# Performance work log

Measured on AMD Instinct MI355X. Metric: run time of the kernel, lower is better.

## Reference

```python
import jax, jax.numpy as jnp
import numpy as np

B, N, F, C = 8, 4096, 1024, 64


def setup_inputs() -> dict:
    key = jax.random.key(0)
    k1, k2, k3 = jax.random.split(key, 3)
    x1 = jax.random.normal(k1, (B, N, F), dtype=jnp.float32)
    x2 = jax.random.normal(k2, (B, N, F), dtype=jnp.float32)
    W = jax.random.normal(k3, (C, F), dtype=jnp.float32) / np.sqrt(F)
    b = jnp.zeros((C,), dtype=jnp.float32)
    return {"x1": x1, "x2": x2, "W": W, "b": b}


def _select_max(x, W, b):
    # x: [B, N, F] -> scores [B, N, C]
    scores = jnp.einsum("bnf,cf->bnc", x, W) + b
    # per-batch, per-class index of max-scoring instance: [B, C]
    idx = jnp.argmax(scores, axis=1)
    # gather the selected instance feature vectors: [B, C, F]
    return jnp.take_along_axis(x, idx[:, :, None], axis=1)


def reference(x1, x2, W, b):
    d = _select_max(x1, W, b)
    d1 = _select_max(x2, W, b)
    return (d, d1)
```

## Files before the change

kernel.cpp:

```cpp
#include <hip/hip_runtime.h>

#define B_   8
#define N_   4096
#define F_   1024
#define C_   64
#define TN   128
#define KC   64
#define NB   (N_ / TN)
#define MARGIN 0.02f

typedef __attribute__((ext_vector_type(8))) short bhalf8;
typedef __attribute__((ext_vector_type(4))) float f32x4;
typedef __attribute__((ext_vector_type(4))) unsigned short us4;

__device__ __forceinline__ unsigned short f2bf_rne(float x) {
    unsigned u = __builtin_bit_cast(unsigned, x);
    u += 0x7fffu + ((u >> 16) & 1u);
    return (unsigned short)(u >> 16);
}
__device__ __forceinline__ float bf2f(unsigned short h) {
    unsigned u = ((unsigned)h) << 16;
    return __builtin_bit_cast(float, u);
}

#define LEXGT(a, ai, b, bi) ((a) > (b) || ((a) == (b) && (ai) < (bi)))
#define INSERT3(vv, nn)                                                   \
    do {                                                                  \
        float _v = (vv); int _n = (nn);                                   \
        if (LEXGT(_v, _n, v0, i0)) { v2=v1; i2=i1; v1=v0; i1=i0; v0=_v; i0=_n; } \
        else if (LEXGT(_v, _n, v1, i1)) { v2=v1; i2=i1; v1=_v; i1=_n; }   \
        else if (LEXGT(_v, _n, v2, i2)) { v2=_v; i2=_n; }                 \
    } while (0)

__global__ __launch_bounds__(256, 2) void score_top3_kernel(
    const float* __restrict__ x1, const float* __restrict__ x2,
    const float* __restrict__ W,
    float* __restrict__ pv, int* __restrict__ pi)
{
    __shared__ __align__(16) char lds[49152];
    __shared__ float tv[4][C_][3];
    __shared__ int   ti[4][C_][3];

    const int tid  = threadIdx.x;
    const int nb   = blockIdx.x;
    const int b    = blockIdx.y;
    const int inp  = blockIdx.z;
    const int n0   = nb * TN;
    const float* __restrict__ x = inp ? x2 : x1;
    const float* __restrict__ xbase = x + ((size_t)b * N_ + n0) * F_;

    const int lane = tid & 63;
    const int w    = tid >> 6;
    const int rsel = lane & 15;
    const int g    = lane >> 4;
    const int swz  = (rsel & 7) << 4;

    f32x4 acc[2][4];
    #pragma unroll
    for (int mt = 0; mt < 2; ++mt)
        #pragma unroll
        for (int nt = 0; nt < 4; ++nt) acc[mt][nt] = (f32x4){0.f, 0.f, 0.f, 0.f};

    for (int kc = 0; kc < F_ / KC; ++kc) {
        const int f0 = kc * KC;
        float4 xv[8], wv[4];
        #pragma unroll
        for (int j = 0; j < 8; ++j) {
            int li = tid + 256 * j, row = li >> 4, fq = li & 15;
            xv[j] = *(const float4*)(xbase + (size_t)row * F_ + f0 + fq * 4);
        }
        #pragma unroll
        for (int j = 0; j < 4; ++j) {
            int li = tid + 256 * j, c = li >> 4, fq = li & 15;
            wv[j] = *(const float4*)(W + (size_t)c * F_ + f0 + fq * 4);
        }
        #pragma unroll
        for (int j = 0; j < 8; ++j) {
            int li = tid + 256 * j, row = li >> 4, fq = li & 15;
            float f[4] = {xv[j].x, xv[j].y, xv[j].z, xv[j].w};
            us4 hh, ll;
            #pragma unroll
            for (int e = 0; e < 4; ++e) {
                unsigned short h = f2bf_rne(f[e]);
                hh[e] = h;
                ll[e] = f2bf_rne(f[e] - bf2f(h));
            }
            int off = (row * 128 + fq * 8) ^ ((row & 7) << 4);
            *(us4*)(lds + off)         = hh;
            *(us4*)(lds + 16384 + off) = ll;
        }
        #pragma unroll
        for (int j = 0; j < 4; ++j) {
            int li = tid + 256 * j, c = li >> 4, fq = li & 15;
            float f[4] = {wv[j].x, wv[j].y, wv[j].z, wv[j].w};
            us4 hh, ll;
            #pragma unroll
            for (int e = 0; e < 4; ++e) {
                unsigned short h = f2bf_rne(f[e]);
                hh[e] = h;
                ll[e] = f2bf_rne(f[e] - bf2f(h));
            }
            int off = (c * 128 + fq * 8) ^ ((c & 7) << 4);
            *(us4*)(lds + 32768 + off) = hh;
            *(us4*)(lds + 40960 + off) = ll;
        }
        __syncthreads();

        #pragma unroll
        for (int ks = 0; ks < 2; ++ks) {
            bhalf8 ah[2], al[2], bh[4], bl[4];
            #pragma unroll
            for (int mt = 0; mt < 2; ++mt) {
                int arow = w * 32 + mt * 16 + rsel;
                int off = (arow * 128 + ks * 64 + g * 16) ^ swz;
                ah[mt] = *(const bhalf8*)(lds + off);
                al[mt] = *(const bhalf8*)(lds + 16384 + off);
            }
            #pragma unroll
            for (int nt = 0; nt < 4; ++nt) {
                int brow = nt * 16 + rsel;
                int off = (brow * 128 + ks * 64 + g * 16) ^ swz;
                bh[nt] = *(const bhalf8*)(lds + 32768 + off);
                bl[nt] = *(const bhalf8*)(lds + 40960 + off);
            }
            #pragma unroll
            for (int mt = 0; mt < 2; ++mt)
                #pragma unroll
                for (int nt = 0; nt < 4; ++nt) {
                    acc[mt][nt] = __builtin_amdgcn_mfma_f32_16x16x32_bf16(ah[mt], bh[nt], acc[mt][nt], 0, 0, 0);
                    acc[mt][nt] = __builtin_amdgcn_mfma_f32_16x16x32_bf16(ah[mt], bl[nt], acc[mt][nt], 0, 0, 0);
                    acc[mt][nt] = __builtin_amdgcn_mfma_f32_16x16x32_bf16(al[mt], bh[nt], acc[mt][nt], 0, 0, 0);
                }
        }
        __syncthreads();
    }

    #pragma unroll
    for (int nt = 0; nt < 4; ++nt) {
        float v0 = -3.4e38f, v1 = -3.4e38f, v2 = -3.4e38f;
        int   i0 = 0x7fffffff, i1 = 0x7fffffff, i2 = 0x7fffffff;
        #pragma unroll
        for (int mt = 0; mt < 2; ++mt)
            #pragma unroll
            for (int r = 0; r < 4; ++r) {
                int n = n0 + w * 32 + mt * 16 + 4 * g + r;
                INSERT3(acc[mt][nt][r], n);
            }
        #pragma unroll
        for (int d = 16; d <= 32; d <<= 1) {
            float u0 = __shfl_xor(v0, d), u1 = __shfl_xor(v1, d), u2 = __shfl_xor(v2, d);
            int   j0 = __shfl_xor(i0, d), j1 = __shfl_xor(i1, d), j2 = __shfl_xor(i2, d);
            INSERT3(u0, j0); INSERT3(u1, j1); INSERT3(u2, j2);
        }
        if (lane < 16) {
            int c = nt * 16 + lane;
            tv[w][c][0] = v0; tv[w][c][1] = v1; tv[w][c][2] = v2;
            ti[w][c][0] = i0; ti[w][c][1] = i1; ti[w][c][2] = i2;
        }
    }
    __syncthreads();

    if (tid < C_) {
        int c = tid;
        float v0 = tv[0][c][0], v1 = tv[0][c][1], v2 = tv[0][c][2];
        int   i0 = ti[0][c][0], i1 = ti[0][c][1], i2 = ti[0][c][2];
        #pragma unroll
        for (int ww = 1; ww < 4; ++ww) {
            INSERT3(tv[ww][c][0], ti[ww][c][0]);
            INSERT3(tv[ww][c][1], ti[ww][c][1]);
            INSERT3(tv[ww][c][2], ti[ww][c][2]);
        }
        int blk = ((inp * B_ + b) * NB + nb);
        pv[(blk * C_ + c) * 3 + 0] = v0; pi[(blk * C_ + c) * 3 + 0] = i0;
        pv[(blk * C_ + c) * 3 + 1] = v1; pi[(blk * C_ + c) * 3 + 1] = i1;
        pv[(blk * C_ + c) * 3 + 2] = v2; pi[(blk * C_ + c) * 3 + 2] = i2;
    }
}

__global__ __launch_bounds__(256) void select_gather_kernel(
    const float* __restrict__ x1, const float* __restrict__ x2,
    const float* __restrict__ W,
    const float* __restrict__ pv, const int* __restrict__ pi,
    float* __restrict__ out)
{
    const int c   = blockIdx.x;
    const int b   = blockIdx.y;
    const int inp = blockIdx.z;
    const int tid = threadIdx.x;

    __shared__ int   s_cnt;
    __shared__ int   s_cand[8];
    __shared__ float s_val[8];
    __shared__ float s_wsum[4];
    __shared__ int   s_win;

    if (tid == 0) s_cnt = 0;
    __syncthreads();

    if (tid < 64) {
        float m = -3.4e38f;
        if (tid < 32) {
            int blk = ((inp * B_ + b) * NB + tid);
            m = pv[(blk * C_ + c) * 3 + 0];
        }
        #pragma unroll
        for (int d = 32; d; d >>= 1) m = fmaxf(m, __shfl_xor(m, d));
        if (tid < 32) {
            int blk = ((inp * B_ + b) * NB + tid);
            #pragma unroll
            for (int k = 0; k < 3; ++k) {
                float v = pv[(blk * C_ + c) * 3 + k];
                if (v >= m - MARGIN) {
                    int p = atomicAdd(&s_cnt, 1);
                    if (p < 8) s_cand[p] = pi[(blk * C_ + c) * 3 + k];
                }
            }
        }
    }
    __syncthreads();

    const float* __restrict__ x = inp ? x2 : x1;
    const int ncand = min(s_cnt, 8);
    int winner;
    if (ncand == 1) {
        winner = s_cand[0];
    } else {
        for (int k = 0; k < ncand; ++k) {
            int n = s_cand[k];
            float4 xv = *(const float4*)(x + ((size_t)b * N_ + n) * F_ + tid * 4);
            float4 wv = *(const float4*)(W + (size_t)c * F_ + tid * 4);
            float p = xv.x * wv.x + xv.y * wv.y + xv.z * wv.z + xv.w * wv.w;
            #pragma unroll
            for (int d = 32; d; d >>= 1) p += __shfl_down(p, d);
            if ((tid & 63) == 0) s_wsum[tid >> 6] = p;
            __syncthreads();
            if (tid == 0) s_val[k] = s_wsum[0] + s_wsum[1] + s_wsum[2] + s_wsum[3];
            __syncthreads();
        }
        if (tid == 0) {
            float bv = s_val[0]; int bn = s_cand[0];
            for (int k = 1; k < ncand; ++k)
                if (s_val[k] > bv || (s_val[k] == bv && s_cand[k] < bn)) { bv = s_val[k]; bn = s_cand[k]; }
            s_win = bn;
        }
        __syncthreads();
        winner = s_win;
    }

    float4 v = *(const float4*)(x + ((size_t)b * N_ + winner) * F_ + tid * 4);
    *(float4*)(out + (((size_t)inp * B_ + b) * C_ + c) * F_ + tid * 4) = v;
}

extern "C" void kernel_launch(void* const* d_in, const int* in_sizes, int n_in,
                              void* d_out, int out_size, void* d_ws, size_t ws_size,
                              hipStream_t stream) {
    const float* x1 = (const float*)d_in[0];
    const float* x2 = (const float*)d_in[1];
    const float* W  = (const float*)d_in[2];

    float* pv = (float*)d_ws;
    int*   pi = (int*)((char*)d_ws + (size_t)2 * B_ * NB * C_ * 3 * sizeof(float));

    dim3 g1(NB, B_, 2);
    score_top3_kernel<<<g1, 256, 0, stream>>>(x1, x2, W, pv, pi);
    dim3 g2(C_, B_, 2);
    select_gather_kernel<<<g2, 256, 0, stream>>>(x1, x2, W, pv, pi, (float*)d_out);
}
```

Baseline: 70.95 us.

## Precompute split-bf16 W, halve row tile, prefetch next x chunk in registers

Adds a small pre-kernel that converts W into hi/lo bf16 arrays once, so the score kernel reads B fragments straight from global memory instead of converting and staging W in LDS for every block. The row tile drops from 128 to 64 and LDS shrinks to 32 KB, allowing 4 blocks per CU. The next K-chunk of x is loaded into registers while the current MFMAs run, overlapping global loads with compute. Per-block candidates drop from top-3 to top-2, which relies on the smaller tile to keep candidate recall. The cost is an extra kernel launch and W fragment reads from global or cache in every block.

```diff
diff --git a/kernel.cpp b/kernel.cpp
--- a/kernel.cpp
+++ b/kernel.cpp
@@ -4,7 +4,7 @@
 #define N_   4096
 #define F_   1024
 #define C_   64
-#define TN   128
+#define TN   64
 #define KC   64
 #define NB   (N_ / TN)
 #define MARGIN 0.02f
@@ -24,22 +24,37 @@
 }
 
 #define LEXGT(a, ai, b, bi) ((a) > (b) || ((a) == (b) && (ai) < (bi)))
-#define INSERT3(vv, nn)                                                   \
+#define INSERT2(vv, nn)                                                   \
     do {                                                                  \
         float _v = (vv); int _n = (nn);                                   \
-        if (LEXGT(_v, _n, v0, i0)) { v2=v1; i2=i1; v1=v0; i1=i0; v0=_v; i0=_n; } \
-        else if (LEXGT(_v, _n, v1, i1)) { v2=v1; i2=i1; v1=_v; i1=_n; }   \
-        else if (LEXGT(_v, _n, v2, i2)) { v2=_v; i2=_n; }                 \
+        if (LEXGT(_v, _n, v0, i0)) { v1=v0; i1=i0; v0=_v; i0=_n; }        \
+        else if (LEXGT(_v, _n, v1, i1)) { v1=_v; i1=_n; }                 \
     } while (0)
 
-__global__ __launch_bounds__(256, 2) void score_top3_kernel(
+__global__ __launch_bounds__(256) void wconv_kernel(
+    const float* __restrict__ W,
+    unsigned short* __restrict__ Wh, unsigned short* __restrict__ Wl)
+{
+    int i = blockIdx.x * 256 + threadIdx.x;
+    float4 v = ((const float4*)W)[i];
+    float f[4] = {v.x, v.y, v.z, v.w};
+    us4 hh, ll;
+    #pragma unroll
+    for (int e = 0; e < 4; ++e) {
+        unsigned short h = f2bf_rne(f[e]);
+        hh[e] = h;
+        ll[e] = f2bf_rne(f[e] - bf2f(h));
+    }
+    ((us4*)Wh)[i] = hh;
+    ((us4*)Wl)[i] = ll;
+}
+
+__global__ __launch_bounds__(256, 4) void score_top2_kernel(
     const float* __restrict__ x1, const float* __restrict__ x2,
-    const float* __restrict__ W,
+    const unsigned short* __restrict__ Wh, const unsigned short* __restrict__ Wl,
     float* __restrict__ pv, int* __restrict__ pi)
 {
-    __shared__ __align__(16) char lds[49152];
-    __shared__ float tv[4][C_][3];
-    __shared__ int   ti[4][C_][3];
+    __shared__ __align__(16) char lds[32768];
 
     const int tid  = threadIdx.x;
     const int nb   = blockIdx.x;
@@ -55,27 +70,20 @@
     const int g    = lane >> 4;
     const int swz  = (rsel & 7) << 4;
 
-    f32x4 acc[2][4];
-    #pragma unroll
-    for (int mt = 0; mt < 2; ++mt)
-        #pragma unroll
-        for (int nt = 0; nt < 4; ++nt) acc[mt][nt] = (f32x4){0.f, 0.f, 0.f, 0.f};
+    f32x4 acc[4];
+    #pragma unroll
+    for (int nt = 0; nt < 4; ++nt) acc[nt] = (f32x4){0.f, 0.f, 0.f, 0.f};
+
+    float4 xv[4];
+    #pragma unroll
+    for (int j = 0; j < 4; ++j) {
+        int li = tid + 256 * j, row = li >> 4, fq = li & 15;
+        xv[j] = *(const float4*)(xbase + (size_t)row * F_ + fq * 4);
+    }
 
     for (int kc = 0; kc < F_ / KC; ++kc) {
-        const int f0 = kc * KC;
-        float4 xv[8], wv[4];
-        #pragma unroll
-        for (int j = 0; j < 8; ++j) {
-            int li = tid + 256 * j, row = li >> 4, fq = li & 15;
-            xv[j] = *(const float4*)(xbase + (size_t)row * F_ + f0 + fq * 4);
-        }
         #pragma unroll
         for (int j = 0; j < 4; ++j) {
-            int li = tid + 256 * j, c = li >> 4, fq = li & 15;
-            wv[j] = *(const float4*)(W + (size_t)c * F_ + f0 + fq * 4);
-        }
-        #pragma unroll
-        for (int j = 0; j < 8; ++j) {
             int li = tid + 256 * j, row = li >> 4, fq = li & 15;
             float f[4] = {xv[j].x, xv[j].y, xv[j].z, xv[j].w};
             us4 hh, ll;
@@ -89,91 +97,81 @@
             *(us4*)(lds + off)         = hh;
             *(us4*)(lds + 16384 + off) = ll;
         }
-        #pragma unroll
-        for (int j = 0; j < 4; ++j) {
-            int li = tid + 256 * j, c = li >> 4, fq = li & 15;
-            float f[4] = {wv[j].x, wv[j].y, wv[j].z, wv[j].w};
-            us4 hh, ll;
-            #pragma unroll
-            for (int e = 0; e < 4; ++e) {
-                unsigned short h = f2bf_rne(f[e]);
-                hh[e] = h;
-                ll[e] = f2bf_rne(f[e] - bf2f(h));
-            }
-            int off = (c * 128 + fq * 8) ^ ((c & 7) << 4);
-            *(us4*)(lds + 32768 + off) = hh;
-            *(us4*)(lds + 40960 + off) = ll;
-        }
         __syncthreads();
 
+        bhalf8 ah[2], al[2];
         #pragma unroll
         for (int ks = 0; ks < 2; ++ks) {
-            bhalf8 ah[2], al[2], bh[4], bl[4];
-            #pragma unroll
-            for (int mt = 0; mt < 2; ++mt) {
-                int arow = w * 32 + mt * 16 + rsel;
-                int off = (arow * 128 + ks * 64 + g * 16) ^ swz;
-                ah[mt] = *(const bhalf8*)(lds + off);
-                al[mt] = *(const bhalf8*)(lds + 16384 + off);
-            }
+            int arow = w * 16 + rsel;
+            int off = (arow * 128 + ks * 64 + g * 16) ^ swz;
+            ah[ks] = *(const bhalf8*)(lds + off);
+            al[ks] = *(const bhalf8*)(lds + 16384 + off);
+        }
+        bhalf8 bh[2][4], bl[2][4];
+        #pragma unroll
+        for (int ks = 0; ks < 2; ++ks)
             #pragma unroll
             for (int nt = 0; nt < 4; ++nt) {
-                int brow = nt * 16 + rsel;
-                int off = (brow * 128 + ks * 64 + g * 16) ^ swz;
-                bh[nt] = *(const bhalf8*)(lds + 32768 + off);
-                bl[nt] = *(const bhalf8*)(lds + 40960 + off);
-            }
-            #pragma unroll
-            for (int mt = 0; mt < 2; ++mt)
-                #pragma unroll
-                for (int nt = 0; nt < 4; ++nt) {
-                    acc[mt][nt] = __builtin_amdgcn_mfma_f32_16x16x32_bf16(ah[mt], bh[nt], acc[mt][nt], 0, 0, 0);
-                    acc[mt][nt] = __builtin_amdgcn_mfma_f32_16x16x32_bf16(ah[mt], bl[nt], acc[mt][nt], 0, 0, 0);
-                    acc[mt][nt] = __builtin_amdgcn_mfma_f32_16x16x32_bf16(al[mt], bh[nt], acc[mt][nt], 0, 0, 0);
-                }
-        }
+                size_t off = (size_t)(nt * 16 + rsel) * F_ + kc * KC + ks * 32 + g * 8;
+                bh[ks][nt] = *(const bhalf8*)(Wh + off);
+                bl[ks][nt] = *(const bhalf8*)(Wl + off);
+            }
+        if (kc + 1 < F_ / KC) {
+            const int f0 = (kc + 1) * KC;
+            #pragma unroll
+            for (int j = 0; j < 4; ++j) {
+                int li = tid + 256 * j, row = li >> 4, fq = li & 15;
+                xv[j] = *(const float4*)(xbase + (size_t)row * F_ + f0 + fq * 4);
+            }
+        }
+        #pragma unroll
+        for (int ks = 0; ks < 2; ++ks)
+            #pragma unroll
+            for (int nt = 0; nt < 4; ++nt) {
+                acc[nt] = __builtin_amdgcn_mfma_f32_16x16x32_bf16(ah[ks], bh[ks][nt], acc[nt], 0, 0, 0);
+                acc[nt] = __builtin_amdgcn_mfma_f32_16x16x32_bf16(ah[ks], bl[ks][nt], acc[nt], 0, 0, 0);
+                acc[nt] = __builtin_amdgcn_mfma_f32_16x16x32_bf16(al[ks], bh[ks][nt], acc[nt], 0, 0, 0);
+            }
         __syncthreads();
     }
 
+    float* tv = (float*)lds;
+    int*   ti = (int*)(lds + 8192);
     #pragma unroll
     for (int nt = 0; nt < 4; ++nt) {
-        float v0 = -3.4e38f, v1 = -3.4e38f, v2 = -3.4e38f;
-        int   i0 = 0x7fffffff, i1 = 0x7fffffff, i2 = 0x7fffffff;
-        #pragma unroll
-        for (int mt = 0; mt < 2; ++mt)
-            #pragma unroll
-            for (int r = 0; r < 4; ++r) {
-                int n = n0 + w * 32 + mt * 16 + 4 * g + r;
-                INSERT3(acc[mt][nt][r], n);
-            }
+        float v0 = -3.4e38f, v1 = -3.4e38f;
+        int   i0 = 0x7fffffff, i1 = 0x7fffffff;
+        #pragma unroll
+        for (int r = 0; r < 4; ++r) {
+            int n = n0 + w * 16 + 4 * g + r;
+            INSERT2(acc[nt][r], n);
+        }
         #pragma unroll
         for (int d = 16; d <= 32; d <<= 1) {
-            float u0 = __shfl_xor(v0, d), u1 = __shfl_xor(v1, d), u2 = __shfl_xor(v2, d);
-            int   j0 = __shfl_xor(i0, d), j1 = __shfl_xor(i1, d), j2 = __shfl_xor(i2, d);
-            INSERT3(u0, j0); INSERT3(u1, j1); INSERT3(u2, j2);
+            float u0 = __shfl_xor(v0, d), u1 = __shfl_xor(v1, d);
+            int   j0 = __shfl_xor(i0, d), j1 = __shfl_xor(i1, d);
+            INSERT2(u0, j0); INSERT2(u1, j1);
         }
         if (lane < 16) {
             int c = nt * 16 + lane;
-            tv[w][c][0] = v0; tv[w][c][1] = v1; tv[w][c][2] = v2;
-            ti[w][c][0] = i0; ti[w][c][1] = i1; ti[w][c][2] = i2;
+            tv[(w * C_ + c) * 2 + 0] = v0; tv[(w * C_ + c) * 2 + 1] = v1;
+            ti[(w * C_ + c) * 2 + 0] = i0; ti[(w * C_ + c) * 2 + 1] = i1;
         }
     }
     __syncthreads();
 
     if (tid < C_) {
         int c = tid;
-        float v0 = tv[0][c][0], v1 = tv[0][c][1], v2 = tv[0][c][2];
-        int   i0 = ti[0][c][0], i1 = ti[0][c][1], i2 = ti[0][c][2];
+        float v0 = tv[(0 * C_ + c) * 2 + 0], v1 = tv[(0 * C_ + c) * 2 + 1];
+        int   i0 = ti[(0 * C_ + c) * 2 + 0], i1 = ti[(0 * C_ + c) * 2 + 1];
         #pragma unroll
         for (int ww = 1; ww < 4; ++ww) {
-            INSERT3(tv[ww][c][0], ti[ww][c][0]);
-            INSERT3(tv[ww][c][1], ti[ww][c][1]);
-            INSERT3(tv[ww][c][2], ti[ww][c][2]);
+            INSERT2(tv[(ww * C_ + c) * 2 + 0], ti[(ww * C_ + c) * 2 + 0]);
+            INSERT2(tv[(ww * C_ + c) * 2 + 1], ti[(ww * C_ + c) * 2 + 1]);
         }
         int blk = ((inp * B_ + b) * NB + nb);
-        pv[(blk * C_ + c) * 3 + 0] = v0; pi[(blk * C_ + c) * 3 + 0] = i0;
-        pv[(blk * C_ + c) * 3 + 1] = v1; pi[(blk * C_ + c) * 3 + 1] = i1;
-        pv[(blk * C_ + c) * 3 + 2] = v2; pi[(blk * C_ + c) * 3 + 2] = i2;
+        pv[(blk * C_ + c) * 2 + 0] = v0; pi[(blk * C_ + c) * 2 + 0] = i0;
+        pv[(blk * C_ + c) * 2 + 1] = v1; pi[(blk * C_ + c) * 2 + 1] = i1;
     }
 }
 
@@ -198,22 +196,16 @@
     __syncthreads();
 
     if (tid < 64) {
-        float m = -3.4e38f;
-        if (tid < 32) {
-            int blk = ((inp * B_ + b) * NB + tid);
-            m = pv[(blk * C_ + c) * 3 + 0];
-        }
+        int blk = ((inp * B_ + b) * NB + tid);
+        float m = pv[(blk * C_ + c) * 2 + 0];
         #pragma unroll
         for (int d = 32; d; d >>= 1) m = fmaxf(m, __shfl_xor(m, d));
-        if (tid < 32) {
-            int blk = ((inp * B_ + b) * NB + tid);
-            #pragma unroll
-            for (int k = 0; k < 3; ++k) {
-                float v = pv[(blk * C_ + c) * 3 + k];
-                if (v >= m - MARGIN) {
-                    int p = atomicAdd(&s_cnt, 1);
-                    if (p < 8) s_cand[p] = pi[(blk * C_ + c) * 3 + k];
-                }
+        #pragma unroll
+        for (int k = 0; k < 2; ++k) {
+            float v = pv[(blk * C_ + c) * 2 + k];
+            if (v >= m - MARGIN) {
+                int p = atomicAdd(&s_cnt, 1);
+                if (p < 8) s_cand[p] = pi[(blk * C_ + c) * 2 + k];
             }
         }
     }
@@ -258,11 +250,14 @@
     const float* x2 = (const float*)d_in[1];
     const float* W  = (const float*)d_in[2];
 
-    float* pv = (float*)d_ws;
-    int*   pi = (int*)((char*)d_ws + (size_t)2 * B_ * NB * C_ * 3 * sizeof(float));
-
+    unsigned short* Wh = (unsigned short*)d_ws;
+    unsigned short* Wl = Wh + (size_t)C_ * F_;
+    float* pv = (float*)((char*)d_ws + 2 * (size_t)C_ * F_ * sizeof(unsigned short));
+    int*   pi = (int*)((char*)pv + (size_t)2 * B_ * NB * C_ * 2 * sizeof(float));
+
+    wconv_kernel<<<C_ * F_ / 1024, 256, 0, stream>>>(W, Wh, Wl);
     dim3 g1(NB, B_, 2);
-    score_top3_kernel<<<g1, 256, 0, stream>>>(x1, x2, W, pv, pi);
+    score_top2_kernel<<<g1, 256, 0, stream>>>(x1, x2, Wh, Wl, pv, pi);
     dim3 g2(C_, B_, 2);
     select_gather_kernel<<<g2, 256, 0, stream>>>(x1, x2, W, pv, pi, (float*)d_out);
 }
```

Result: slower. 145.1 us (+104.6%).
